# Kernel optimization log

Hardware: AMD Instinct MI355X
Metric: run time of the kernel (lower is better)

The kernel has to match this reference:

```python
import jax, jax.numpy as jnp
import numpy as np

B, IN_DIM, D, P = 256, 1024, 512, 2048


def setup_inputs() -> dict:
    key = jax.random.key(0)
    ks = jax.random.split(key, 7)
    return {
        "x": jax.random.normal(ks[0], (B, IN_DIM), dtype=jnp.float32),
        "y": jax.random.randint(ks[1], (B,), 0, P),
        "Wb": jax.random.normal(ks[2], (D, IN_DIM), dtype=jnp.float32) * 0.02,
        "bb": jax.random.normal(ks[3], (D,), dtype=jnp.float32) * 0.02,
        "Wm": jax.random.normal(ks[4], (P, D), dtype=jnp.float32) * 0.02,
        "bm": jax.random.normal(ks[5], (P,), dtype=jnp.float32) * 0.02,
        "proxies": jax.random.normal(ks[6], (P, D), dtype=jnp.float32),
    }


def reference(x, y, Wb, bb, Wm, bm, proxies):
    # backbone: Linear(in_dim -> D)
    feat = x @ Wb.T + bb                         # [B, D]
    # L2-norm regularizer: mean of per-row L2 norms
    reg_e = jnp.mean(jnp.sqrt(jnp.sum(feat * feat, axis=1)))
    # multi: classification head Linear(D -> P)
    out = feat @ Wm.T + bm                       # [B, P]
    # squared euclidean distance to each proxy (broadcast diff + square + sum)
    den = jnp.sum((feat[:, None, :] - proxies[None, :, :]) ** 2, axis=2)  # [B, P]
    # cross-entropy on negated distances
    logp = jax.nn.log_softmax(-den, axis=1)      # [B, P]
    loss = -jnp.mean(jnp.take_along_axis(logp, y[:, None], axis=1))
    return out, loss, reg_e
```

## Files before the change

kernel.cpp:

```cpp
#include <hip/hip_runtime.h>
#include <hip/hip_bf16.h>
#include <math.h>

#define NB   256
#define KIN  1024
#define ND   512
#define NP   2048
#define NTOT 4096

typedef __bf16 bf16x8 __attribute__((ext_vector_type(8)));
typedef float  f32x4  __attribute__((ext_vector_type(4)));
typedef unsigned short ush8 __attribute__((ext_vector_type(8)));

#define OFF_WPB    0u
#define OFF_FEATB  4194304u
#define OFF_PN2    4456448u
#define OFF_LOGITS 4464640u
#define OFF_ROWLP  6561792u
#define OFF_ROWNM  6562816u

__device__ __forceinline__ float bf2f(unsigned short h) {
    union { unsigned u; float f; } v; v.u = ((unsigned)h) << 16; return v.f;
}

__device__ __forceinline__ ush8 pack8(float4 f0, float4 f1) {
    union { ush8 v; __hip_bfloat162 h[4]; } o;
    o.h[0] = __float22bfloat162_rn(make_float2(f0.x, f0.y));
    o.h[1] = __float22bfloat162_rn(make_float2(f0.z, f0.w));
    o.h[2] = __float22bfloat162_rn(make_float2(f1.x, f1.y));
    o.h[3] = __float22bfloat162_rn(make_float2(f1.z, f1.w));
    return o.v;
}

__device__ __forceinline__ void async16(const unsigned short* g, unsigned short* l) {
    __builtin_amdgcn_global_load_lds(
        (const __attribute__((address_space(1))) unsigned int*)g,
        (__attribute__((address_space(3))) unsigned int*)l, 16, 0, 0);
}

__global__ __launch_bounds__(256) void k_one(
    const float* __restrict__ x, const float* __restrict__ Wb,
    const float* __restrict__ bb, const float* __restrict__ Wm,
    const float* __restrict__ prox, unsigned short* __restrict__ featb,
    unsigned short* __restrict__ WPb, float* __restrict__ pn2)
{
    const int bid = blockIdx.x, t = threadIdx.x;
    const int lane = t & 63, w = t >> 6;
    if (bid < 32) {
        __shared__ unsigned short As[2][64 * 32];
        __shared__ unsigned short Bs[2][64 * 32];
        const int n0 = (bid & 7) * 64, m0 = (bid >> 3) * 64;
        const int srow = t >> 2, sc = (t & 3) * 8;
        const float* gA = x  + (size_t)(m0 + srow) * KIN + sc;
        const float* gB = Wb + (size_t)(n0 + srow) * KIN + sc;
        float4 a0 = *(const float4*)gA, a1 = *(const float4*)(gA + 4);
        float4 b0 = *(const float4*)gB, b1 = *(const float4*)(gB + 4);
        f32x4 acc[2][2] = {};
        const int wm = (w >> 1) * 32, wn = (w & 1) * 32;
        const int arow = wm + (lane & 15), brow = wn + (lane & 15);
        const int fcol = (lane >> 4) * 8;
        for (int ks = 0; ks < KIN / 32; ++ks) {
            *(ush8*)&As[ks & 1][srow * 32 + sc] = pack8(a0, a1);
            *(ush8*)&Bs[ks & 1][srow * 32 + sc] = pack8(b0, b1);
            __syncthreads();
            if (ks + 1 < KIN / 32) {
                a0 = *(const float4*)(gA + (ks + 1) * 32);
                a1 = *(const float4*)(gA + (ks + 1) * 32 + 4);
                b0 = *(const float4*)(gB + (ks + 1) * 32);
                b1 = *(const float4*)(gB + (ks + 1) * 32 + 4);
            }
            const unsigned short* as = &As[ks & 1][0];
            const unsigned short* bs = &Bs[ks & 1][0];
            bf16x8 af0 = *(const bf16x8*)&as[(arow     ) * 32 + fcol];
            bf16x8 af1 = *(const bf16x8*)&as[(arow + 16) * 32 + fcol];
            bf16x8 bf0 = *(const bf16x8*)&bs[(brow     ) * 32 + fcol];
            bf16x8 bf1 = *(const bf16x8*)&bs[(brow + 16) * 32 + fcol];
            acc[0][0] = __builtin_amdgcn_mfma_f32_16x16x32_bf16(af0, bf0, acc[0][0], 0, 0, 0);
            acc[0][1] = __builtin_amdgcn_mfma_f32_16x16x32_bf16(af0, bf1, acc[0][1], 0, 0, 0);
            acc[1][0] = __builtin_amdgcn_mfma_f32_16x16x32_bf16(af1, bf0, acc[1][0], 0, 0, 0);
            acc[1][1] = __builtin_amdgcn_mfma_f32_16x16x32_bf16(af1, bf1, acc[1][1], 0, 0, 0);
        }
        const int q = lane >> 4, cn = lane & 15;
#pragma unroll
        for (int i = 0; i < 2; ++i)
#pragma unroll
            for (int j = 0; j < 2; ++j) {
                const int n = n0 + wn + 16 * j + cn;
                const float bias = bb[n];
#pragma unroll
                for (int r = 0; r < 4; ++r) {
                    const int m = m0 + wm + 16 * i + q * 4 + r;
                    featb[m * ND + n] = __hip_bfloat16_raw(__hip_bfloat16(acc[i][j][r] + bias)).x;
                }
            }
    } else if (bid < 544) {
        const int idx = (bid - 32) * 2048 + t * 8;
        float4 f0 = *(const float4*)(Wm + idx), f1 = *(const float4*)(Wm + idx + 4);
        *(ush8*)(WPb + idx) = pack8(f0, f1);
    } else {
        const int b = bid - 544;
        const int idx = b * 2048 + t * 8;
        float4 f0 = *(const float4*)(prox + idx), f1 = *(const float4*)(prox + idx + 4);
        *(ush8*)(WPb + (size_t)NP * ND + idx) = pack8(f0, f1);
        float s = f0.x*f0.x + f0.y*f0.y + f0.z*f0.z + f0.w*f0.w
                + f1.x*f1.x + f1.y*f1.y + f1.z*f1.z + f1.w*f1.w;
#pragma unroll
        for (int off = 32; off; off >>= 1) s += __shfl_down(s, off);
        if (lane == 0) pn2[b * 4 + w] = s;
    }
}

__global__ __launch_bounds__(256) void k_head(
    const unsigned short* __restrict__ featb, const unsigned short* __restrict__ WPb,
    const float* __restrict__ bm, const float* __restrict__ pn2,
    float* __restrict__ out, float* __restrict__ logits)
{
    __shared__ unsigned short As[2][128 * 32];
    __shared__ unsigned short Bs[2][128 * 32];
    const int t = threadIdx.x, lane = t & 63, w = t >> 6;
    const int n0 = blockIdx.x * 128;
    const int m0 = blockIdx.y * 128;
    const int drow = w * 16 + (lane >> 2), dcol = (lane & 3) * 8;
    const unsigned short* gA0 = featb + (size_t)(m0 +      drow) * ND + dcol;
    const unsigned short* gA1 = featb + (size_t)(m0 + 64 + drow) * ND + dcol;
    const unsigned short* gB0 = WPb   + (size_t)(n0 +      drow) * ND + dcol;
    const unsigned short* gB1 = WPb   + (size_t)(n0 + 64 + drow) * ND + dcol;

#define ISSUE(buf, ks)                                              \
    do {                                                            \
        const int o_ = (ks) * 32;                                   \
        async16(gA0 + o_, &As[buf][(     w * 16) * 32]);            \
        async16(gA1 + o_, &As[buf][(64 + w * 16) * 32]);            \
        async16(gB0 + o_, &Bs[buf][(     w * 16) * 32]);            \
        async16(gB1 + o_, &Bs[buf][(64 + w * 16) * 32]);            \
    } while (0)

    f32x4 acc[4][4] = {};
    const int wm = (w >> 1) * 64, wn = (w & 1) * 64;
    const int fr = lane & 15, fcol = (lane >> 4) * 8;
    ISSUE(0, 0);
    for (int ks = 0; ks < ND / 32; ++ks) {
        __syncthreads();
        if (ks + 1 < ND / 32) ISSUE((ks + 1) & 1, ks + 1);
        const unsigned short* as = &As[ks & 1][0];
        const unsigned short* bs = &Bs[ks & 1][0];
        bf16x8 af[4], bf[4];
#pragma unroll
        for (int i = 0; i < 4; ++i) af[i] = *(const bf16x8*)&as[(wm + 16 * i + fr) * 32 + fcol];
#pragma unroll
        for (int j = 0; j < 4; ++j) bf[j] = *(const bf16x8*)&bs[(wn + 16 * j + fr) * 32 + fcol];
#pragma unroll
        for (int i = 0; i < 4; ++i)
#pragma unroll
            for (int j = 0; j < 4; ++j)
                acc[i][j] = __builtin_amdgcn_mfma_f32_16x16x32_bf16(af[i], bf[j], acc[i][j], 0, 0, 0);
    }
#undef ISSUE
    const bool isProxy = (n0 >= NP);
    const int q = lane >> 4;
#pragma unroll
    for (int i = 0; i < 4; ++i)
#pragma unroll
        for (int j = 0; j < 4; ++j) {
            const int n = n0 + wn + 16 * j + fr;
            const float cadd = isProxy ? pn2[n - NP] : bm[n];
#pragma unroll
            for (int r = 0; r < 4; ++r) {
                const int m = m0 + wm + 16 * i + q * 4 + r;
                const float v = acc[i][j][r];
                if (isProxy) logits[m * NP + (n - NP)] = 2.0f * v - cadd;
                else         out[m * NP + n] = v + cadd;
            }
        }
}

__device__ __forceinline__ float block_reduce(float v, float* sred, int op)
{
    const int lane = threadIdx.x & 63, wave = threadIdx.x >> 6;
#pragma unroll
    for (int off = 32; off; off >>= 1) {
        float o = __shfl_down(v, off);
        v = op ? fmaxf(v, o) : (v + o);
    }
    if (lane == 0) sred[wave] = v;
    __syncthreads();
    if (threadIdx.x == 0) {
        float r = sred[0];
#pragma unroll
        for (int wv = 1; wv < 4; ++wv) r = op ? fmaxf(r, sred[wv]) : (r + sred[wv]);
        sred[0] = r;
    }
    __syncthreads();
    float r = sred[0];
    __syncthreads();
    return r;
}

__global__ __launch_bounds__(256) void k_loss(
    const unsigned short* __restrict__ featb, const float* __restrict__ logits,
    const int* __restrict__ y, float* __restrict__ rowlp, float* __restrict__ rownm)
{
    __shared__ float sred[4];
    const int b = blockIdx.x, t = threadIdx.x;

    float s = 0.f;
#pragma unroll
    for (int c = 0; c < 2; ++c) {
        float v = bf2f(featb[b * ND + t * 2 + c]); s += v * v;
    }
    float fn2 = block_reduce(s, sred, 0);

    const float* lr = logits + (size_t)b * NP;
    float lv[8], mx = -INFINITY;
#pragma unroll
    for (int j = 0; j < 8; ++j) { lv[j] = lr[t + 256 * j]; mx = fmaxf(mx, lv[j]); }
    float MX = block_reduce(mx, sred, 1);
    float es = 0.f;
#pragma unroll
    for (int j = 0; j < 8; ++j) es += __expf(lv[j] - MX);
    float SUM = block_reduce(es, sred, 0);

    if (t == 0) {
        float ly = lr[y[b]];
        rowlp[b] = ly - MX - __logf(SUM);
        rownm[b] = sqrtf(fn2);
    }
}

__global__ __launch_bounds__(256) void k_final(
    const float* __restrict__ rowlp, const float* __restrict__ rownm,
    float* __restrict__ tail)
{
    __shared__ float sred[4];
    const int t = threadIdx.x;
    float s1 = block_reduce(rowlp[t], sred, 0);
    float s2 = block_reduce(rownm[t], sred, 0);
    if (t == 0) {
        tail[0] = -s1 / (float)NB;
        tail[1] =  s2 / (float)NB;
    }
}

extern "C" void kernel_launch(void* const* d_in, const int* in_sizes, int n_in,
                              void* d_out, int out_size, void* d_ws, size_t ws_size,
                              hipStream_t stream)
{
    const float* x       = (const float*)d_in[0];
    const int*   y       = (const int*)  d_in[1];
    const float* Wb      = (const float*)d_in[2];
    const float* bb      = (const float*)d_in[3];
    const float* Wm      = (const float*)d_in[4];
    const float* bm      = (const float*)d_in[5];
    const float* proxies = (const float*)d_in[6];

    char* ws = (char*)d_ws;
    unsigned short* WPb    = (unsigned short*)(ws + OFF_WPB);
    unsigned short* featb  = (unsigned short*)(ws + OFF_FEATB);
    float*          pn2    = (float*)(ws + OFF_PN2);
    float*          logits = (float*)(ws + OFF_LOGITS);
    float*          rowlp  = (float*)(ws + OFF_ROWLP);
    float*          rownm  = (float*)(ws + OFF_ROWNM);

    float* out  = (float*)d_out;
    float* tail = out + (size_t)NB * NP;

    k_one <<<dim3(1056), dim3(256), 0, stream>>>(x, Wb, bb, Wm, proxies, featb, WPb, pn2);
    k_head<<<dim3(NTOT / 128, NB / 128), dim3(256), 0, stream>>>(featb, WPb, bm, pn2, out, logits);
    k_loss<<<dim3(NB), dim3(256), 0, stream>>>(featb, logits, y, rowlp, rownm);
    k_final<<<dim3(1), dim3(256), 0, stream>>>(rowlp, rownm, tail);
}
```

Before: 112.3 us.

## Fuse all stages into one persistent kernel with software grid barriers

Replaces the four launches with a single 256-block kernel that separates the backbone GEMM/conversion, head GEMM, per-row loss and final reduction phases with atomic-counter grid barriers. The head GEMM tile shrinks to 64x64 so that 256 blocks cover the whole output, and the final sums use atomics into a small buffer that is cleared with a memset. The aim is to remove launch gaps and the separate final kernel. In exchange it adds spin-wait barriers, relies on all 256 blocks being co-resident, and uses smaller head tiles with less reuse.

```diff
diff --git a/kernel.cpp b/kernel.cpp
--- a/kernel.cpp
+++ b/kernel.cpp
@@ -16,8 +16,7 @@
 #define OFF_FEATB  4194304u
 #define OFF_PN2    4456448u
 #define OFF_LOGITS 4464640u
-#define OFF_ROWLP  6561792u
-#define OFF_ROWNM  6562816u
+#define OFF_SYNC   6561792u
 
 __device__ __forceinline__ float bf2f(unsigned short h) {
     union { unsigned u; float f; } v; v.u = ((unsigned)h) << 16; return v.f;
@@ -38,17 +37,57 @@
         (__attribute__((address_space(3))) unsigned int*)l, 16, 0, 0);
 }
 
-__global__ __launch_bounds__(256) void k_one(
-    const float* __restrict__ x, const float* __restrict__ Wb,
-    const float* __restrict__ bb, const float* __restrict__ Wm,
-    const float* __restrict__ prox, unsigned short* __restrict__ featb,
-    unsigned short* __restrict__ WPb, float* __restrict__ pn2)
+__device__ __forceinline__ void gridbar(unsigned* bar, int idx) {
+    __syncthreads();
+    if (threadIdx.x == 0) {
+        __threadfence();
+        __hip_atomic_fetch_add(&bar[idx], 1u, __ATOMIC_RELAXED, __HIP_MEMORY_SCOPE_AGENT);
+        while (__hip_atomic_load(&bar[idx], __ATOMIC_RELAXED, __HIP_MEMORY_SCOPE_AGENT) < 256u)
+            __builtin_amdgcn_s_sleep(2);
+        __threadfence();
+    }
+    __syncthreads();
+}
+
+__device__ __forceinline__ float block_reduce(float v, float* sred, int op)
 {
+    const int lane = threadIdx.x & 63, wave = threadIdx.x >> 6;
+#pragma unroll
+    for (int off = 32; off; off >>= 1) {
+        float o = __shfl_down(v, off);
+        v = op ? fmaxf(v, o) : (v + o);
+    }
+    if (lane == 0) sred[wave] = v;
+    __syncthreads();
+    if (threadIdx.x == 0) {
+        float r = sred[0];
+#pragma unroll
+        for (int wv = 1; wv < 4; ++wv) r = op ? fmaxf(r, sred[wv]) : (r + sred[wv]);
+        sred[0] = r;
+    }
+    __syncthreads();
+    float r = sred[0];
+    __syncthreads();
+    return r;
+}
+
+__global__ __launch_bounds__(256) void k_all(
+    const float* __restrict__ x, const int* __restrict__ y,
+    const float* __restrict__ Wb, const float* __restrict__ bb,
+    const float* __restrict__ Wm, const float* __restrict__ bm,
+    const float* __restrict__ prox,
+    unsigned short* __restrict__ featb, unsigned short* __restrict__ WPb,
+    float* __restrict__ pn2, float* __restrict__ logits,
+    unsigned* __restrict__ bar, float* __restrict__ accum,
+    float* __restrict__ out, float* __restrict__ tail)
+{
+    __shared__ unsigned short As[2][64 * 32];
+    __shared__ unsigned short Bs[2][64 * 32];
+    __shared__ float sred[4];
     const int bid = blockIdx.x, t = threadIdx.x;
     const int lane = t & 63, w = t >> 6;
+
     if (bid < 32) {
-        __shared__ unsigned short As[2][64 * 32];
-        __shared__ unsigned short Bs[2][64 * 32];
         const int n0 = (bid & 7) * 64, m0 = (bid >> 3) * 64;
         const int srow = t >> 2, sc = (t & 3) * 8;
         const float* gA = x  + (size_t)(m0 + srow) * KIN + sc;
@@ -79,6 +118,7 @@
             acc[0][1] = __builtin_amdgcn_mfma_f32_16x16x32_bf16(af0, bf1, acc[0][1], 0, 0, 0);
             acc[1][0] = __builtin_amdgcn_mfma_f32_16x16x32_bf16(af1, bf0, acc[1][0], 0, 0, 0);
             acc[1][1] = __builtin_amdgcn_mfma_f32_16x16x32_bf16(af1, bf1, acc[1][1], 0, 0, 0);
+            __syncthreads();
         }
         const int q = lane >> 4, cn = lane & 15;
 #pragma unroll
@@ -93,151 +133,106 @@
                     featb[m * ND + n] = __hip_bfloat16_raw(__hip_bfloat16(acc[i][j][r] + bias)).x;
                 }
             }
-    } else if (bid < 544) {
-        const int idx = (bid - 32) * 2048 + t * 8;
-        float4 f0 = *(const float4*)(Wm + idx), f1 = *(const float4*)(Wm + idx + 4);
-        *(ush8*)(WPb + idx) = pack8(f0, f1);
     } else {
-        const int b = bid - 544;
-        const int idx = b * 2048 + t * 8;
-        float4 f0 = *(const float4*)(prox + idx), f1 = *(const float4*)(prox + idx + 4);
-        *(ush8*)(WPb + (size_t)NP * ND + idx) = pack8(f0, f1);
-        float s = f0.x*f0.x + f0.y*f0.y + f0.z*f0.z + f0.w*f0.w
-                + f1.x*f1.x + f1.y*f1.y + f1.z*f1.z + f1.w*f1.w;
-#pragma unroll
-        for (int off = 32; off; off >>= 1) s += __shfl_down(s, off);
-        if (lane == 0) pn2[b * 4 + w] = s;
-    }
-}
-
-__global__ __launch_bounds__(256) void k_head(
-    const unsigned short* __restrict__ featb, const unsigned short* __restrict__ WPb,
-    const float* __restrict__ bm, const float* __restrict__ pn2,
-    float* __restrict__ out, float* __restrict__ logits)
-{
-    __shared__ unsigned short As[2][128 * 32];
-    __shared__ unsigned short Bs[2][128 * 32];
-    const int t = threadIdx.x, lane = t & 63, w = t >> 6;
-    const int n0 = blockIdx.x * 128;
-    const int m0 = blockIdx.y * 128;
-    const int drow = w * 16 + (lane >> 2), dcol = (lane & 3) * 8;
-    const unsigned short* gA0 = featb + (size_t)(m0 +      drow) * ND + dcol;
-    const unsigned short* gA1 = featb + (size_t)(m0 + 64 + drow) * ND + dcol;
-    const unsigned short* gB0 = WPb   + (size_t)(n0 +      drow) * ND + dcol;
-    const unsigned short* gB1 = WPb   + (size_t)(n0 + 64 + drow) * ND + dcol;
-
-#define ISSUE(buf, ks)                                              \
-    do {                                                            \
-        const int o_ = (ks) * 32;                                   \
-        async16(gA0 + o_, &As[buf][(     w * 16) * 32]);            \
-        async16(gA1 + o_, &As[buf][(64 + w * 16) * 32]);            \
-        async16(gB0 + o_, &Bs[buf][(     w * 16) * 32]);            \
-        async16(gB1 + o_, &Bs[buf][(64 + w * 16) * 32]);            \
-    } while (0)
-
-    f32x4 acc[4][4] = {};
-    const int wm = (w >> 1) * 64, wn = (w & 1) * 64;
-    const int fr = lane & 15, fcol = (lane >> 4) * 8;
-    ISSUE(0, 0);
-    for (int ks = 0; ks < ND / 32; ++ks) {
-        __syncthreads();
-        if (ks + 1 < ND / 32) ISSUE((ks + 1) & 1, ks + 1);
-        const unsigned short* as = &As[ks & 1][0];
-        const unsigned short* bs = &Bs[ks & 1][0];
-        bf16x8 af[4], bf[4];
-#pragma unroll
-        for (int i = 0; i < 4; ++i) af[i] = *(const bf16x8*)&as[(wm + 16 * i + fr) * 32 + fcol];
-#pragma unroll
-        for (int j = 0; j < 4; ++j) bf[j] = *(const bf16x8*)&bs[(wn + 16 * j + fr) * 32 + fcol];
-#pragma unroll
-        for (int i = 0; i < 4; ++i)
-#pragma unroll
-            for (int j = 0; j < 4; ++j)
-                acc[i][j] = __builtin_amdgcn_mfma_f32_16x16x32_bf16(af[i], bf[j], acc[i][j], 0, 0, 0);
-    }
+        const int gw = (bid - 32) * 4 + w;
+        for (int r = gw; r < NTOT; r += 896) {
+            const float* src = (r < NP) ? (Wm + (size_t)r * ND) : (prox + (size_t)(r - NP) * ND);
+            float4 v0 = *(const float4*)(src + lane * 8);
+            float4 v1 = *(const float4*)(src + lane * 8 + 4);
+            *(ush8*)(WPb + (size_t)r * ND + lane * 8) = pack8(v0, v1);
+            if (r >= NP) {
+                float s = v0.x*v0.x + v0.y*v0.y + v0.z*v0.z + v0.w*v0.w
+                        + v1.x*v1.x + v1.y*v1.y + v1.z*v1.z + v1.w*v1.w;
+#pragma unroll
+                for (int off = 32; off; off >>= 1) s += __shfl_down(s, off);
+                if (lane == 0) pn2[r - NP] = s;
+            }
+        }
+    }
+    gridbar(bar, 0);
+
+    {
+        const int n0 = (bid & 63) * 64;
+        const int m0 = (bid >> 6) * 64;
+        const int drow = w * 16 + (lane >> 2), dcol = (lane & 3) * 8;
+        const unsigned short* gA = featb + (size_t)(m0 + drow) * ND + dcol;
+        const unsigned short* gB = WPb   + (size_t)(n0 + drow) * ND + dcol;
+#define ISSUE(buf, ks)                                        \
+        do {                                                  \
+            async16(gA + (ks) * 32, &As[buf][(w * 16) * 32]); \
+            async16(gB + (ks) * 32, &Bs[buf][(w * 16) * 32]); \
+        } while (0)
+        f32x4 acc[2][2] = {};
+        const int wm = (w >> 1) * 32, wn = (w & 1) * 32;
+        const int fr = lane & 15, fcol = (lane >> 4) * 8;
+        ISSUE(0, 0);
+        for (int ks = 0; ks < ND / 32; ++ks) {
+            __syncthreads();
+            if (ks + 1 < ND / 32) ISSUE((ks + 1) & 1, ks + 1);
+            const unsigned short* as = &As[ks & 1][0];
+            const unsigned short* bs = &Bs[ks & 1][0];
+            bf16x8 af0 = *(const bf16x8*)&as[(wm      + fr) * 32 + fcol];
+            bf16x8 af1 = *(const bf16x8*)&as[(wm + 16 + fr) * 32 + fcol];
+            bf16x8 bf0 = *(const bf16x8*)&bs[(wn      + fr) * 32 + fcol];
+            bf16x8 bf1 = *(const bf16x8*)&bs[(wn + 16 + fr) * 32 + fcol];
+            acc[0][0] = __builtin_amdgcn_mfma_f32_16x16x32_bf16(af0, bf0, acc[0][0], 0, 0, 0);
+            acc[0][1] = __builtin_amdgcn_mfma_f32_16x16x32_bf16(af0, bf1, acc[0][1], 0, 0, 0);
+            acc[1][0] = __builtin_amdgcn_mfma_f32_16x16x32_bf16(af1, bf0, acc[1][0], 0, 0, 0);
+            acc[1][1] = __builtin_amdgcn_mfma_f32_16x16x32_bf16(af1, bf1, acc[1][1], 0, 0, 0);
+            __syncthreads();
+        }
 #undef ISSUE
-    const bool isProxy = (n0 >= NP);
-    const int q = lane >> 4;
-#pragma unroll
-    for (int i = 0; i < 4; ++i)
-#pragma unroll
-        for (int j = 0; j < 4; ++j) {
-            const int n = n0 + wn + 16 * j + fr;
-            const float cadd = isProxy ? pn2[n - NP] : bm[n];
-#pragma unroll
-            for (int r = 0; r < 4; ++r) {
-                const int m = m0 + wm + 16 * i + q * 4 + r;
-                const float v = acc[i][j][r];
-                if (isProxy) logits[m * NP + (n - NP)] = 2.0f * v - cadd;
-                else         out[m * NP + n] = v + cadd;
-            }
-        }
-}
-
-__device__ __forceinline__ float block_reduce(float v, float* sred, int op)
-{
-    const int lane = threadIdx.x & 63, wave = threadIdx.x >> 6;
-#pragma unroll
-    for (int off = 32; off; off >>= 1) {
-        float o = __shfl_down(v, off);
-        v = op ? fmaxf(v, o) : (v + o);
-    }
-    if (lane == 0) sred[wave] = v;
-    __syncthreads();
-    if (threadIdx.x == 0) {
-        float r = sred[0];
-#pragma unroll
-        for (int wv = 1; wv < 4; ++wv) r = op ? fmaxf(r, sred[wv]) : (r + sred[wv]);
-        sred[0] = r;
-    }
-    __syncthreads();
-    float r = sred[0];
-    __syncthreads();
-    return r;
-}
-
-__global__ __launch_bounds__(256) void k_loss(
-    const unsigned short* __restrict__ featb, const float* __restrict__ logits,
-    const int* __restrict__ y, float* __restrict__ rowlp, float* __restrict__ rownm)
-{
-    __shared__ float sred[4];
-    const int b = blockIdx.x, t = threadIdx.x;
-
-    float s = 0.f;
-#pragma unroll
-    for (int c = 0; c < 2; ++c) {
-        float v = bf2f(featb[b * ND + t * 2 + c]); s += v * v;
-    }
-    float fn2 = block_reduce(s, sred, 0);
-
-    const float* lr = logits + (size_t)b * NP;
-    float lv[8], mx = -INFINITY;
-#pragma unroll
-    for (int j = 0; j < 8; ++j) { lv[j] = lr[t + 256 * j]; mx = fmaxf(mx, lv[j]); }
-    float MX = block_reduce(mx, sred, 1);
-    float es = 0.f;
-#pragma unroll
-    for (int j = 0; j < 8; ++j) es += __expf(lv[j] - MX);
-    float SUM = block_reduce(es, sred, 0);
-
-    if (t == 0) {
-        float ly = lr[y[b]];
-        rowlp[b] = ly - MX - __logf(SUM);
-        rownm[b] = sqrtf(fn2);
-    }
-}
-
-__global__ __launch_bounds__(256) void k_final(
-    const float* __restrict__ rowlp, const float* __restrict__ rownm,
-    float* __restrict__ tail)
-{
-    __shared__ float sred[4];
-    const int t = threadIdx.x;
-    float s1 = block_reduce(rowlp[t], sred, 0);
-    float s2 = block_reduce(rownm[t], sred, 0);
-    if (t == 0) {
-        tail[0] = -s1 / (float)NB;
-        tail[1] =  s2 / (float)NB;
+        const bool isProxy = (n0 >= NP);
+        const int q = lane >> 4;
+#pragma unroll
+        for (int i = 0; i < 2; ++i)
+#pragma unroll
+            for (int j = 0; j < 2; ++j) {
+                const int n = n0 + wn + 16 * j + fr;
+                const float cadd = isProxy ? pn2[n - NP] : bm[n];
+#pragma unroll
+                for (int r = 0; r < 4; ++r) {
+                    const int m = m0 + wm + 16 * i + q * 4 + r;
+                    const float v = acc[i][j][r];
+                    if (isProxy) logits[m * NP + (n - NP)] = 2.0f * v - cadd;
+                    else         out[m * NP + n] = v + cadd;
+                }
+            }
+    }
+    gridbar(bar, 1);
+
+    {
+        const int b = bid;
+        float s = 0.f;
+#pragma unroll
+        for (int c = 0; c < 2; ++c) {
+            float v = bf2f(featb[b * ND + t * 2 + c]); s += v * v;
+        }
+        float fn2 = block_reduce(s, sred, 0);
+
+        const float* lr = logits + (size_t)b * NP;
+        float lv[8], mx = -INFINITY;
+#pragma unroll
+        for (int j = 0; j < 8; ++j) { lv[j] = lr[t + 256 * j]; mx = fmaxf(mx, lv[j]); }
+        float MX = block_reduce(mx, sred, 1);
+        float es = 0.f;
+#pragma unroll
+        for (int j = 0; j < 8; ++j) es += __expf(lv[j] - MX);
+        float SUM = block_reduce(es, sred, 0);
+
+        if (t == 0) {
+            float ly = lr[y[b]];
+            atomicAdd(&accum[0], ly - MX - __logf(SUM));
+            atomicAdd(&accum[1], sqrtf(fn2));
+        }
+    }
+    gridbar(bar, 2);
+
+    if (bid == 0 && t == 0) {
+        float s0 = __hip_atomic_load(&accum[0], __ATOMIC_RELAXED, __HIP_MEMORY_SCOPE_AGENT);
+        float s1 = __hip_atomic_load(&accum[1], __ATOMIC_RELAXED, __HIP_MEMORY_SCOPE_AGENT);
+        tail[0] = -s0 / (float)NB;
+        tail[1] =  s1 / (float)NB;
     }
 }
 
@@ -258,14 +253,14 @@
     unsigned short* featb  = (unsigned short*)(ws + OFF_FEATB);
     float*          pn2    = (float*)(ws + OFF_PN2);
     float*          logits = (float*)(ws + OFF_LOGITS);
-    float*          rowlp  = (float*)(ws + OFF_ROWLP);
-    float*          rownm  = (float*)(ws + OFF_ROWNM);
+    unsigned*       bar    = (unsigned*)(ws + OFF_SYNC);
+    float*          accum  = (float*)(ws + OFF_SYNC + 16);
 
     float* out  = (float*)d_out;
     float* tail = out + (size_t)NB * NP;
 
-    k_one <<<dim3(1056), dim3(256), 0, stream>>>(x, Wb, bb, Wm, proxies, featb, WPb, pn2);
-    k_head<<<dim3(NTOT / 128, NB / 128), dim3(256), 0, stream>>>(featb, WPb, bm, pn2, out, logits);
-    k_loss<<<dim3(NB), dim3(256), 0, stream>>>(featb, logits, y, rowlp, rownm);
-    k_final<<<dim3(1), dim3(256), 0, stream>>>(rowlp, rownm, tail);
-}
+    hipMemsetAsync(ws + OFF_SYNC, 0, 64, stream);
+    k_all<<<dim3(256), dim3(256), 0, stream>>>(
+        x, y, Wb, bb, Wm, bm, proxies,
+        featb, WPb, pn2, logits, bar, accum, out, tail);
+}
```

After: 151.5 us. +34.9%, slower.
